# Kernel tuning notes

Measured on AMD Instinct MI355X. Metric: run time of the kernel, lower is better.

The kernel has to match this reference:

```python
import jax, jax.numpy as jnp
import numpy as np

H = 4
NEG_SLOPE = 0.2
N_P, N_A = 100000, 100000
E = 500000
L = 200000
F_IN, F_HID, F_OUT = 128, 128, 64


def setup_inputs() -> dict:
    key = jax.random.key(0)
    ks = jax.random.split(key, 32)
    s = 0.1  # weight init scale
    inp = {
        'x_paper': jax.random.normal(ks[0], (N_P, F_IN), jnp.float32),
        'x_author': jax.random.normal(ks[1], (N_A, F_IN), jnp.float32),
        'ei_pa': jax.random.randint(ks[2], (2, E), 0, N_P, jnp.int32),
        'ei_ap': jax.random.randint(ks[3], (2, E), 0, N_A, jnp.int32),
        'edge_label_index': jax.random.randint(ks[4], (2, L), 0, N_P, jnp.int32),
        # layer 1 params
        'p1W': s * jax.random.normal(ks[5], (F_IN, F_HID), jnp.float32),
        'p1b': jnp.zeros((F_HID,), jnp.float32),
        'a1W': s * jax.random.normal(ks[6], (F_IN, F_HID), jnp.float32),
        'a1b': jnp.zeros((F_HID,), jnp.float32),
        's1pa': s * jax.random.normal(ks[7], (H, F_HID // H), jnp.float32),
        'd1pa': s * jax.random.normal(ks[8], (H, F_HID // H), jnp.float32),
        's1ap': s * jax.random.normal(ks[9], (H, F_HID // H), jnp.float32),
        'd1ap': s * jax.random.normal(ks[10], (H, F_HID // H), jnp.float32),
        'k1W': s * jax.random.normal(ks[11], (F_HID, F_HID), jnp.float32),
        'k1b': jnp.zeros((F_HID,), jnp.float32),
        'q1': s * jax.random.normal(ks[12], (F_HID,), jnp.float32),
        # layer 2 params
        'p2W': s * jax.random.normal(ks[13], (F_HID, F_OUT), jnp.float32),
        'p2b': jnp.zeros((F_OUT,), jnp.float32),
        'a2W': s * jax.random.normal(ks[14], (F_HID, F_OUT), jnp.float32),
        'a2b': jnp.zeros((F_OUT,), jnp.float32),
        's2pa': s * jax.random.normal(ks[15], (H, F_OUT // H), jnp.float32),
        'd2pa': s * jax.random.normal(ks[16], (H, F_OUT // H), jnp.float32),
        's2ap': s * jax.random.normal(ks[17], (H, F_OUT // H), jnp.float32),
        'd2ap': s * jax.random.normal(ks[18], (H, F_OUT // H), jnp.float32),
        'k2W': s * jax.random.normal(ks[19], (F_OUT, F_OUT), jnp.float32),
        'k2b': jnp.zeros((F_OUT,), jnp.float32),
        'q2': s * jax.random.normal(ks[20], (F_OUT,), jnp.float32),
    }
    return inp


def _edge_attn(h_src, h_dst, src, dst, a_src, a_dst, num_dst):
    # h_*: [N, H, D]; a_*: [H, D]. Per-edge node-level GAT-style attention.
    alpha = (jnp.einsum('nhd,hd->nh', h_src, a_src)[src]
             + jnp.einsum('nhd,hd->nh', h_dst, a_dst)[dst])  # [E, H]
    alpha = jnp.where(alpha >= 0, alpha, NEG_SLOPE * alpha)  # leaky_relu
    amax = jax.ops.segment_max(alpha, dst, num_segments=num_dst)
    amax = jnp.where(jnp.isfinite(amax), amax, 0.0)
    ex = jnp.exp(alpha - amax[dst])
    denom = jax.ops.segment_sum(ex, dst, num_segments=num_dst)
    w = ex / (denom[dst] + 1e-16)
    out = jax.ops.segment_sum(h_src[src] * w[:, :, None], dst, num_segments=num_dst)
    return jax.nn.relu(out).reshape(num_dst, -1)  # [N_dst, H*D]


def _group(xs, q, kW, kb):
    # Semantic-level attention over metapaths (PyG HANConv `group`).
    out = jnp.stack(xs)  # [M, N, F]
    score = (q * jnp.tanh(out @ kW + kb).mean(axis=1)).sum(-1)  # [M]
    attn = jax.nn.softmax(score)
    return (attn[:, None, None] * out).sum(0)


def _han_layer(x_p, x_a, ei_pa, ei_ap, pW, pb, aW, ab, s_pa, d_pa, s_ap, d_ap, kW, kb, q):
    D = pW.shape[1] // H
    h_p = (x_p @ pW + pb).reshape(-1, H, D)
    h_a = (x_a @ aW + ab).reshape(-1, H, D)
    out_a = _edge_attn(h_p, h_a, ei_pa[0], ei_pa[1], s_pa, d_pa, h_a.shape[0])
    out_p = _edge_attn(h_a, h_p, ei_ap[0], ei_ap[1], s_ap, d_ap, h_p.shape[0])
    z_p = _group([out_p], q, kW, kb)
    z_a = _group([out_a], q, kW, kb)
    return z_p, z_a


def reference(x_paper, x_author, ei_pa, ei_ap, edge_label_index,
              p1W, p1b, a1W, a1b, s1pa, d1pa, s1ap, d1ap, k1W, k1b, q1,
              p2W, p2b, a2W, a2b, s2pa, d2pa, s2ap, d2ap, k2W, k2b, q2):
    z_p, z_a = _han_layer(x_paper, x_author, ei_pa, ei_ap,
                          p1W, p1b, a1W, a1b, s1pa, d1pa, s1ap, d1ap, k1W, k1b, q1)
    z_p, z_a = _han_layer(z_p, z_a, ei_pa, ei_ap,
                          p2W, p2b, a2W, a2b, s2pa, d2pa, s2ap, d2ap, k2W, k2b, q2)
    src = z_p[edge_label_index[0]]
    dst = z_a[edge_label_index[1]]
    return (src * dst).sum(axis=-1)  # [L]
```

## Files before the change

kernel.cpp:

```cpp
#include <hip/hip_runtime.h>


#define HEADS 4

typedef _Float16 f16x8 __attribute__((ext_vector_type(8)));
typedef _Float16 f16x4 __attribute__((ext_vector_type(4)));
typedef float    f32x4 __attribute__((ext_vector_type(4)));

__device__ __forceinline__ float leaky02(float a) {
    return a >= 0.f ? a : 0.2f * a;
}

__device__ __forceinline__ void prep_one(const float* W, _Float16* Wf, int M, int o) {
    const int v = o & 7, lane = (o >> 3) & 63, rest = o >> 9;
    const int jl = rest & 3, t = (rest >> 2) & 3, grp = rest >> 4;
    const int k = t * 32 + (lane >> 4) * 8 + v;
    const int n = (grp * 4 + jl) * 16 + (lane & 15);
    Wf[o] = (_Float16)W[k * M + n];
}

__global__ __launch_bounds__(256) void prep_w4(
    const float* __restrict__ W1, _Float16* __restrict__ Wf1,
    const float* __restrict__ W2, _Float16* __restrict__ Wf2,
    const float* __restrict__ W3, _Float16* __restrict__ Wf3,
    const float* __restrict__ W4, _Float16* __restrict__ Wf4) {
    int o = blockIdx.x * 256 + threadIdx.x;
    if (o < 16384)       prep_one(W1, Wf1, 128, o);
    else if (o < 32768)  prep_one(W2, Wf2, 128, o - 16384);
    else if (o < 40960)  prep_one(W3, Wf3, 64, o - 32768);
    else if (o < 49152)  prep_one(W4, Wf4, 64, o - 40960);
}

template<int M, bool AHALF>
__global__ __launch_bounds__(256) void gemm_mfma_dual(
    const void* __restrict__ XA, const _Float16* __restrict__ WfA,
    const float* __restrict__ bA, _Float16* __restrict__ outA,
    const float* __restrict__ svA, const float* __restrict__ dvA,
    float* __restrict__ asA, float* __restrict__ adA,
    const void* __restrict__ XB, const _Float16* __restrict__ WfB,
    const float* __restrict__ bB, _Float16* __restrict__ outB,
    const float* __restrict__ svB, const float* __restrict__ dvB,
    float* __restrict__ asB, float* __restrict__ adB,
    int N, int nbs) {
    constexpr int NSPLIT = (M == 128) ? 2 : 1;
    constexpr int JT  = 4;
    constexpr int D   = M / HEADS;
    constexpr int HPB = 64 / D;
    constexpr int HL  = 4 / HPB;
    constexpr int SA  = 136;
    constexpr int WFH = JT * 4 * 64 * 8;
    __shared__ _Float16 lds_a[64 * SA];
    __shared__ _Float16 lds_w[WFH];

    const bool second = blockIdx.x >= (unsigned)nbs;
    const void* __restrict__ X      = second ? XB : XA;
    const _Float16* __restrict__ Wf = second ? WfB : WfA;
    const float* __restrict__ b     = second ? bB : bA;
    _Float16* __restrict__ out      = second ? outB : outA;
    const float* __restrict__ sv    = second ? svB : svA;
    const float* __restrict__ dv    = second ? dvB : dvA;
    float* __restrict__ asb         = second ? asB : asA;
    float* __restrict__ adb         = second ? adB : adA;
    const int b0    = second ? blockIdx.x - nbs : blockIdx.x;
    const int brow  = b0 / NSPLIT;
    const int split = b0 % NSPLIT;
    const int row0  = brow * 64;
    const int colb  = split * 64;

    const int wave = threadIdx.x >> 6;
    const int lane = threadIdx.x & 63;
    const int m    = lane & 15;
    const int quad = lane >> 4;

    {
        const _Float16* wsrc = Wf + split * WFH;
        const int base = threadIdx.x * 8;
        #pragma unroll
        for (int it = 0; it < WFH / 2048; ++it) {
            f16x8 v = *(const f16x8*)(wsrc + it * 2048 + base);
            *(f16x8*)(lds_w + it * 2048 + base) = v;
        }
    }
    if (AHALF) {
        #pragma unroll
        for (int it = 0; it < 4; ++it) {
            const int r = it * 16 + (threadIdx.x >> 4);
            const int k = (threadIdx.x & 15) * 8;
            int gr = row0 + r; if (gr >= N) gr = N - 1;
            f16x8 v = *(const f16x8*)((const _Float16*)X + (size_t)gr * 128 + k);
            *(f16x8*)(lds_a + r * SA + k) = v;
        }
    } else {
        #pragma unroll
        for (int it = 0; it < 8; ++it) {
            const int r = it * 8 + (threadIdx.x >> 5);
            const int k = (threadIdx.x & 31) * 4;
            int gr = row0 + r; if (gr >= N) gr = N - 1;
            float4 v = *(const float4*)((const float*)X + (size_t)gr * 128 + k);
            f16x4 h = {(_Float16)v.x, (_Float16)v.y, (_Float16)v.z, (_Float16)v.w};
            *(f16x4*)(lds_a + r * SA + k) = h;
        }
    }
    __syncthreads();

    f32x4 acc[JT];
    #pragma unroll
    for (int j = 0; j < JT; ++j) acc[j] = (f32x4){0.f, 0.f, 0.f, 0.f};

    const int ab = (wave * 16 + m) * SA;
    #pragma unroll
    for (int t = 0; t < 4; ++t) {
        f16x8 a = *(const f16x8*)(lds_a + ab + t * 32 + quad * 8);
        #pragma unroll
        for (int j = 0; j < JT; ++j) {
            f16x8 bf = *(const f16x8*)(lds_w + ((t * JT + j) * 64 + lane) * 8);
            acc[j] = __builtin_amdgcn_mfma_f32_16x16x32_f16(a, bf, acc[j], 0, 0, 0);
        }
    }

    #pragma unroll
    for (int j = 0; j < JT; ++j) {
        const float bias = b[colb + j * 16 + m];
        #pragma unroll
        for (int r = 0; r < 4; ++r)
            lds_a[(wave * 16 + quad * 4 + r) * SA + j * 16 + m] =
                (_Float16)(acc[j][r] + bias);
    }

    {
        const int r = lane >> 2;
        const int q = lane & 3;
        float ps = 0.f, pd = 0.f;
        #pragma unroll
        for (int j = 0; j < 4; ++j) {
            f16x4 v4 = *(const f16x4*)(&lds_a[(wave * 16 + r) * SA + q * 16 + 4 * j]);
            float4 s4 = *(const float4*)(sv + colb + q * 16 + 4 * j);
            float4 d4 = *(const float4*)(dv + colb + q * 16 + 4 * j);
            const float v0 = (float)v4[0], v1 = (float)v4[1],
                        v2 = (float)v4[2], v3 = (float)v4[3];
            ps += v0 * s4.x + v1 * s4.y + v2 * s4.z + v3 * s4.w;
            pd += v0 * d4.x + v1 * d4.y + v2 * d4.z + v3 * d4.w;
        }
        if (HL == 2) { ps += __shfl_xor(ps, 1); pd += __shfl_xor(pd, 1); }
        const int grow = row0 + wave * 16 + r;
        if (grow < N && (q & (HL - 1)) == 0) {
            const int hh = split * HPB + q / HL;
            asb[(size_t)grow * HEADS + hh] = ps;
            adb[(size_t)grow * HEADS + hh] = pd;
        }
    }

    {
        const int lr = lane & 15;
        const int rq = lane >> 4;
        #pragma unroll
        for (int i = 0; i < 4; ++i) {
            const int lrow = i * 4 + rq;
            const int grow = row0 + wave * 16 + lrow;
            if (grow < N) {
                f16x4 v = *(const f16x4*)(&lds_a[(wave * 16 + lrow) * SA + lr * 4]);
                *(f16x4*)(out + (size_t)grow * M + colb + lr * 4) = v;
            }
        }
    }
}

__global__ __launch_bounds__(256) void hist_dual(
    const int* __restrict__ dst_pa, const int* __restrict__ dst_ap,
    int* __restrict__ counts, int N, int E) {
    const int eg = blockIdx.x * 256 + threadIdx.x;
    if (eg >= 2 * E) return;
    const int idx = (eg < E) ? dst_pa[eg] : (N + dst_ap[eg - E]);
    atomicAdd(counts + idx, 1);
}

__global__ __launch_bounds__(256) void scan_blk(
    const int* __restrict__ in, int* __restrict__ out,
    int* __restrict__ bsum, int N) {
    __shared__ int sh[256];
    const int base = blockIdx.x * 1024 + threadIdx.x * 4;
    int v[4]; int s = 0;
    #pragma unroll
    for (int j = 0; j < 4; ++j) { v[j] = (base + j < N) ? in[base + j] : 0; s += v[j]; }
    sh[threadIdx.x] = s;
    __syncthreads();
    for (int off = 1; off < 256; off <<= 1) {
        int t = (threadIdx.x >= off) ? sh[threadIdx.x - off] : 0;
        __syncthreads();
        sh[threadIdx.x] += t;
        __syncthreads();
    }
    int run = sh[threadIdx.x] - s;
    #pragma unroll
    for (int j = 0; j < 4; ++j) {
        if (base + j < N) out[base + j] = run;
        run += v[j];
    }
    if (threadIdx.x == 255) bsum[blockIdx.x] = sh[255];
}

__global__ __launch_bounds__(256) void scan_sums(int* __restrict__ bsum, int nb) {
    __shared__ int sh[256];
    int v = (threadIdx.x < nb) ? bsum[threadIdx.x] : 0;
    sh[threadIdx.x] = v;
    __syncthreads();
    for (int off = 1; off < 256; off <<= 1) {
        int t = (threadIdx.x >= off) ? sh[threadIdx.x - off] : 0;
        __syncthreads();
        sh[threadIdx.x] += t;
        __syncthreads();
    }
    if (threadIdx.x < nb) bsum[threadIdx.x] = sh[threadIdx.x] - v;
}

__global__ __launch_bounds__(256) void scan_add(
    int* __restrict__ out, const int* __restrict__ bsum, int N) {
    const int base = blockIdx.x * 1024 + threadIdx.x * 4;
    const int add = bsum[blockIdx.x];
    #pragma unroll
    for (int j = 0; j < 4; ++j)
        if (base + j < N) out[base + j] += add;
}

__global__ __launch_bounds__(256) void scatter_dual(
    const int* __restrict__ src_pa, const int* __restrict__ dst_pa,
    const int* __restrict__ src_ap, const int* __restrict__ dst_ap,
    const int* __restrict__ offsets, int* __restrict__ cursor,
    int* __restrict__ perm, int N, int E) {
    const int eg = blockIdx.x * 256 + threadIdx.x;
    if (eg >= 2 * E) return;
    int idx, val;
    if (eg < E) { idx = dst_pa[eg];         val = src_pa[eg]; }
    else        { idx = N + dst_ap[eg - E]; val = src_ap[eg - E]; }
    const int pos = offsets[idx] + atomicAdd(cursor + idx, 1);
    perm[pos] = val;
}

__global__ __launch_bounds__(256) void deg_hist(
    const int* __restrict__ cnt, int* __restrict__ bhist, int n) {
    __shared__ int lh[64];
    if (threadIdx.x < 64) lh[threadIdx.x] = 0;
    __syncthreads();
    for (int i = blockIdx.x * 256 + threadIdx.x; i < n; i += gridDim.x * 256) {
        int c = cnt[i]; if (c > 63) c = 63;
        atomicAdd(&lh[c], 1);
    }
    __syncthreads();
    if (threadIdx.x < 64) atomicAdd(&bhist[threadIdx.x], lh[threadIdx.x]);
}

__global__ __launch_bounds__(256) void deg_scatter(
    const int* __restrict__ cnt, int* __restrict__ bcur,
    int* __restrict__ order, int n) {
    __shared__ int lh[64];
    __shared__ int lbase[64];
    if (threadIdx.x < 64) lh[threadIdx.x] = 0;
    __syncthreads();
    const int i = blockIdx.x * 256 + threadIdx.x;
    int c = 0, lpos = 0;
    if (i < n) {
        c = cnt[i]; if (c > 63) c = 63;
        lpos = atomicAdd(&lh[c], 1);
    }
    __syncthreads();
    if (threadIdx.x < 64 && lh[threadIdx.x] > 0)
        lbase[threadIdx.x] = atomicAdd(&bcur[threadIdx.x], lh[threadIdx.x]);
    __syncthreads();
    if (i < n) order[lbase[c] + lpos] = i;
}

template<int F, int D>
__global__ __launch_bounds__(256) void csr_attn_agg_dual(
    const int* __restrict__ order,
    const int* __restrict__ perm, const int* __restrict__ offsets,
    const int* __restrict__ counts,
    const float* __restrict__ asrcP, const float* __restrict__ adstP,
    const _Float16* __restrict__ hP, _Float16* __restrict__ outA,
    const float* __restrict__ asrcA, const float* __restrict__ adstA,
    const _Float16* __restrict__ hA, _Float16* __restrict__ outP,
    int N) {
    constexpr int LPN = F / 8;
    const int gid  = blockIdx.x * 256 + threadIdx.x;
    const int slotF = gid / LPN;
    const int lane  = gid % LPN;
    if (slotF >= 2 * N) return;
    const int slot = 2 * N - 1 - slotF;
    const int node_g = order[slot];
    const bool second = node_g >= N;
    const int node = second ? node_g - N : node_g;
    const float* __restrict__ asrc    = second ? asrcA : asrcP;
    const float* __restrict__ adst    = second ? adstA : adstP;
    const _Float16* __restrict__ hsrc = second ? hA : hP;
    _Float16* __restrict__ out        = second ? outP : outA;

    const int start = offsets[node_g];
    const int cnt   = counts[node_g];
    const int f0 = lane * 8;
    const int h  = f0 / D;
    const float ad = adst[(size_t)node * HEADS + h];

    float den = 0.f;
    float acc[8];
    #pragma unroll
    for (int j = 0; j < 8; ++j) acc[j] = 0.f;
    const int last = cnt - 1;
    for (int i = 0; i < cnt; i += 4) {
        const int i1 = (i + 1 < cnt) ? i + 1 : last;
        const int i2 = (i + 2 < cnt) ? i + 2 : last;
        const int i3 = (i + 3 < cnt) ? i + 3 : last;
        const int s0 = perm[start + i];
        const int s1 = perm[start + i1];
        const int s2 = perm[start + i2];
        const int s3 = perm[start + i3];
        const float a0 = asrc[(size_t)s0 * HEADS + h];
        const float a1 = asrc[(size_t)s1 * HEADS + h];
        const float a2 = asrc[(size_t)s2 * HEADS + h];
        const float a3 = asrc[(size_t)s3 * HEADS + h];
        f16x8 h0 = *(const f16x8*)(hsrc + (size_t)s0 * F + f0);
        f16x8 h1 = *(const f16x8*)(hsrc + (size_t)s1 * F + f0);
        f16x8 h2 = *(const f16x8*)(hsrc + (size_t)s2 * F + f0);
        f16x8 h3 = *(const f16x8*)(hsrc + (size_t)s3 * F + f0);
        const float e0 = __expf(leaky02(a0 + ad));
        float e1 = __expf(leaky02(a1 + ad));
        float e2 = __expf(leaky02(a2 + ad));
        float e3 = __expf(leaky02(a3 + ad));
        if (i + 1 >= cnt) e1 = 0.f;
        if (i + 2 >= cnt) e2 = 0.f;
        if (i + 3 >= cnt) e3 = 0.f;
        den += (e0 + e1) + (e2 + e3);
        #pragma unroll
        for (int j = 0; j < 8; ++j)
            acc[j] += e0 * (float)h0[j] + e1 * (float)h1[j]
                    + e2 * (float)h2[j] + e3 * (float)h3[j];
    }
    const float inv = 1.f / (den + 1e-16f);
    f16x8 o;
    #pragma unroll
    for (int j = 0; j < 8; ++j)
        o[j] = (_Float16)fmaxf(acc[j] * inv, 0.f);
    *(f16x8*)(out + (size_t)node * F + f0) = o;
}

__global__ __launch_bounds__(256) void edge_dot(
    const int* __restrict__ eli, const _Float16* __restrict__ zp,
    const _Float16* __restrict__ za, float* __restrict__ out, int L) {
    constexpr int LPE = 8;
    const int gid  = blockIdx.x * blockDim.x + threadIdx.x;
    const int e    = gid / LPE;
    const int lane = gid % LPE;
    if (e >= L) return;
    const int p = eli[e], a = eli[(size_t)L + e];
    f16x8 pv = *(const f16x8*)(zp + (size_t)p * 64 + lane * 8);
    f16x8 av = *(const f16x8*)(za + (size_t)a * 64 + lane * 8);
    float s = 0.f;
    #pragma unroll
    for (int j = 0; j < 8; ++j) s += (float)pv[j] * (float)av[j];
    #pragma unroll
    for (int off = 4; off > 0; off >>= 1) s += __shfl_xor(s, off);
    if (lane == 0) out[e] = s;
}

static inline int cdiv(long long a, long long b) { return (int)((a + b - 1) / b); }

extern "C" void kernel_launch(void* const* d_in, const int* in_sizes, int n_in,
                              void* d_out, int out_size, void* d_ws, size_t ws_size,
                              hipStream_t stream) {
    const float* x_p  = (const float*)d_in[0];
    const float* x_a  = (const float*)d_in[1];
    const int* ei_pa  = (const int*)d_in[2];
    const int* ei_ap  = (const int*)d_in[3];
    const int* eli    = (const int*)d_in[4];
    const float* p1W = (const float*)d_in[5];
    const float* p1b = (const float*)d_in[6];
    const float* a1W = (const float*)d_in[7];
    const float* a1b = (const float*)d_in[8];
    const float* s1pa = (const float*)d_in[9];
    const float* d1pa = (const float*)d_in[10];
    const float* s1ap = (const float*)d_in[11];
    const float* d1ap = (const float*)d_in[12];
    const float* p2W = (const float*)d_in[16];
    const float* p2b = (const float*)d_in[17];
    const float* a2W = (const float*)d_in[18];
    const float* a2b = (const float*)d_in[19];
    const float* s2pa = (const float*)d_in[20];
    const float* d2pa = (const float*)d_in[21];
    const float* s2ap = (const float*)d_in[22];
    const float* d2ap = (const float*)d_in[23];

    const int NP = in_sizes[0] / 128;
    const int E  = in_sizes[2] / 2;
    const int L  = in_sizes[4] / 2;
    const int N  = NP;

    char* ws = (char*)d_ws;
    size_t off = 0;
    auto alloc = [&](size_t bytes) -> char* {
        char* p = ws + off;
        off += (bytes + 255) & ~(size_t)255;
        return p;
    };
    _Float16* h_p1   = (_Float16*)alloc((size_t)N * 128 * 2);
    _Float16* h_a1   = (_Float16*)alloc((size_t)N * 128 * 2);
    _Float16* out_p1 = (_Float16*)alloc((size_t)N * 128 * 2);
    _Float16* out_a1 = (_Float16*)alloc((size_t)N * 128 * 2);
    _Float16* h_p2   = (_Float16*)alloc((size_t)N * 64 * 2);
    _Float16* h_a2   = (_Float16*)alloc((size_t)N * 64 * 2);
    _Float16* out_p2 = (_Float16*)alloc((size_t)N * 64 * 2);
    _Float16* out_a2 = (_Float16*)alloc((size_t)N * 64 * 2);
    float* asrc_pa = (float*)alloc((size_t)N * HEADS * 4);
    float* adst_pa = (float*)alloc((size_t)N * HEADS * 4);
    float* asrc_ap = (float*)alloc((size_t)N * HEADS * 4);
    float* adst_ap = (float*)alloc((size_t)N * HEADS * 4);
    _Float16* Wf1p = (_Float16*)alloc(16384 * 2);
    _Float16* Wf1a = (_Float16*)alloc(16384 * 2);
    _Float16* Wf2p = (_Float16*)alloc(8192 * 2);
    _Float16* Wf2a = (_Float16*)alloc(8192 * 2);
    int* cnt2    = (int*)alloc((size_t)2 * N * 4);
    int* cursor2 = (int*)alloc((size_t)2 * N * 4);
    int* bhist   = (int*)alloc(256);
    int* off2    = (int*)alloc((size_t)2 * N * 4);
    int* perm2   = (int*)alloc((size_t)2 * E * 4);
    int* order2  = (int*)alloc((size_t)2 * N * 4);
    int* bsum    = (int*)alloc(256 * 4);

    const int* src_pa = ei_pa;
    const int* dst_pa = ei_pa + E;
    const int* src_ap = ei_ap;
    const int* dst_ap = ei_ap + E;

    const int N2 = 2 * N;
    const int nbScan = cdiv(N2, 1024);

    prep_w4<<<cdiv(49152, 256), 256, 0, stream>>>(p1W, Wf1p, a1W, Wf1a, p2W, Wf2p, a2W, Wf2a);
    hipMemsetAsync(cnt2, 0, ((size_t)4 * N + 64) * 4, stream);
    hist_dual<<<cdiv((long long)2 * E, 256), 256, 0, stream>>>(dst_pa, dst_ap, cnt2, N, E);
    scan_blk<<<nbScan, 256, 0, stream>>>(cnt2, off2, bsum, N2);
    scan_sums<<<1, 256, 0, stream>>>(bsum, nbScan);
    scan_add<<<nbScan, 256, 0, stream>>>(off2, bsum, N2);
    scatter_dual<<<cdiv((long long)2 * E, 256), 256, 0, stream>>>(
        src_pa, dst_pa, src_ap, dst_ap, off2, cursor2, perm2, N, E);
    deg_hist<<<256, 256, 0, stream>>>(cnt2, bhist, N2);
    scan_sums<<<1, 256, 0, stream>>>(bhist, 64);
    deg_scatter<<<cdiv(N2, 256), 256, 0, stream>>>(cnt2, bhist, order2, N2);

    const int nbs1 = cdiv(N, 64) * 2;
    const int nbs2 = cdiv(N, 64);

    gemm_mfma_dual<128, false><<<2 * nbs1, 256, 0, stream>>>(
        x_p, Wf1p, p1b, h_p1, s1pa, d1ap, asrc_pa, adst_ap,
        x_a, Wf1a, a1b, h_a1, s1ap, d1pa, asrc_ap, adst_pa, N, nbs1);
    csr_attn_agg_dual<128, 32><<<cdiv((long long)N2 * 16, 256), 256, 0, stream>>>(
        order2, perm2, off2, cnt2,
        asrc_pa, adst_pa, h_p1, out_a1,
        asrc_ap, adst_ap, h_a1, out_p1, N);

    gemm_mfma_dual<64, true><<<2 * nbs2, 256, 0, stream>>>(
        out_p1, Wf2p, p2b, h_p2, s2pa, d2ap, asrc_pa, adst_ap,
        out_a1, Wf2a, a2b, h_a2, s2ap, d2pa, asrc_ap, adst_pa, N, nbs2);
    csr_attn_agg_dual<64, 16><<<cdiv((long long)N2 * 8, 256), 256, 0, stream>>>(
        order2, perm2, off2, cnt2,
        asrc_pa, adst_pa, h_p2, out_a2,
        asrc_ap, adst_ap, h_a2, out_p2, N);

    edge_dot<<<cdiv((long long)L * 8, 256), 256, 0, stream>>>(
        eli, out_p2, out_a2, (float*)d_out, L);
}
```

Before: 439.5 us.

## Fuse layer-1 attention aggregation with layer-2 projection GEMM in one kernel

Replaces the layer-1 CSR attention aggregation kernel and the layer-2 projection GEMM with a single kernel. Each block aggregates 16 destination nodes, ordered by degree, into LDS, applies ReLU, multiplies by the LDS-resident layer-2 weights with MFMA, and writes h2 plus the per-head source and destination attention logits. This removes the out_p1/out_a1 intermediate round-trip through global memory and one launch. The degree-sort histogram now keeps paper and author nodes in separate buckets so each 16-node group belongs to one graph direction. The risks are load imbalance from the persistent grid-stride loop over groups, lower occupancy from the larger LDS footprint, and new attention-logit buffers.

```diff
diff --git a/kernel.cpp b/kernel.cpp
--- a/kernel.cpp
+++ b/kernel.cpp
@@ -237,36 +237,198 @@
 }
 
 __global__ __launch_bounds__(256) void deg_hist(
-    const int* __restrict__ cnt, int* __restrict__ bhist, int n) {
-    __shared__ int lh[64];
-    if (threadIdx.x < 64) lh[threadIdx.x] = 0;
-    __syncthreads();
-    for (int i = blockIdx.x * 256 + threadIdx.x; i < n; i += gridDim.x * 256) {
+    const int* __restrict__ cnt, int* __restrict__ bhist, int n2) {
+    __shared__ int lh[128];
+    if (threadIdx.x < 128) lh[threadIdx.x] = 0;
+    __syncthreads();
+    const int N = n2 >> 1;
+    for (int i = blockIdx.x * 256 + threadIdx.x; i < n2; i += gridDim.x * 256) {
         int c = cnt[i]; if (c > 63) c = 63;
-        atomicAdd(&lh[c], 1);
-    }
-    __syncthreads();
-    if (threadIdx.x < 64) atomicAdd(&bhist[threadIdx.x], lh[threadIdx.x]);
+        atomicAdd(&lh[(i >= N ? 64 : 0) + c], 1);
+    }
+    __syncthreads();
+    if (threadIdx.x < 128) atomicAdd(&bhist[threadIdx.x], lh[threadIdx.x]);
 }
 
 __global__ __launch_bounds__(256) void deg_scatter(
     const int* __restrict__ cnt, int* __restrict__ bcur,
-    int* __restrict__ order, int n) {
-    __shared__ int lh[64];
-    __shared__ int lbase[64];
-    if (threadIdx.x < 64) lh[threadIdx.x] = 0;
-    __syncthreads();
+    int* __restrict__ order, int n2) {
+    __shared__ int lh[128];
+    __shared__ int lbase[128];
+    if (threadIdx.x < 128) lh[threadIdx.x] = 0;
+    __syncthreads();
+    const int N = n2 >> 1;
     const int i = blockIdx.x * 256 + threadIdx.x;
-    int c = 0, lpos = 0;
-    if (i < n) {
-        c = cnt[i]; if (c > 63) c = 63;
-        lpos = atomicAdd(&lh[c], 1);
-    }
-    __syncthreads();
-    if (threadIdx.x < 64 && lh[threadIdx.x] > 0)
+    int key = 0, lpos = 0;
+    if (i < n2) {
+        int c = cnt[i]; if (c > 63) c = 63;
+        key = (i >= N ? 64 : 0) + c;
+        lpos = atomicAdd(&lh[key], 1);
+    }
+    __syncthreads();
+    if (threadIdx.x < 128 && lh[threadIdx.x] > 0)
         lbase[threadIdx.x] = atomicAdd(&bcur[threadIdx.x], lh[threadIdx.x]);
     __syncthreads();
-    if (i < n) order[lbase[c] + lpos] = i;
+    if (i < n2) order[lbase[key] + lpos] = i;
+}
+
+__global__ __launch_bounds__(256) void agg_proj_dual(
+    const int* __restrict__ order,
+    const int* __restrict__ perm, const int* __restrict__ offsets,
+    const int* __restrict__ counts,
+    const float* __restrict__ as1_0, const float* __restrict__ ad1_0,
+    const _Float16* __restrict__ h1_0,
+    const _Float16* __restrict__ Wf_0, const float* __restrict__ bb_0,
+    _Float16* __restrict__ h2_0,
+    const float* __restrict__ sv_0, const float* __restrict__ dv_0,
+    float* __restrict__ as2_0, float* __restrict__ ad2_0,
+    const float* __restrict__ as1_1, const float* __restrict__ ad1_1,
+    const _Float16* __restrict__ h1_1,
+    const _Float16* __restrict__ Wf_1, const float* __restrict__ bb_1,
+    _Float16* __restrict__ h2_1,
+    const float* __restrict__ sv_1, const float* __restrict__ dv_1,
+    float* __restrict__ as2_1, float* __restrict__ ad2_1,
+    int N, int GB) {
+    constexpr int SAF = 136;
+    constexpr int SH  = 72;
+    __shared__ _Float16 ldsW[8192];
+    __shared__ _Float16 ldsA[16 * SAF];
+    __shared__ _Float16 ldsH[16 * SH];
+
+    const bool d1 = blockIdx.x >= (unsigned)GB;
+    const float*    __restrict__ as1 = d1 ? as1_1 : as1_0;
+    const float*    __restrict__ ad1 = d1 ? ad1_1 : ad1_0;
+    const _Float16* __restrict__ h1  = d1 ? h1_1 : h1_0;
+    const _Float16* __restrict__ Wf  = d1 ? Wf_1 : Wf_0;
+    const float*    __restrict__ bb  = d1 ? bb_1 : bb_0;
+    _Float16*       __restrict__ h2  = d1 ? h2_1 : h2_0;
+    const float*    __restrict__ sv  = d1 ? sv_1 : sv_0;
+    const float*    __restrict__ dv  = d1 ? dv_1 : dv_0;
+    float*          __restrict__ as2 = d1 ? as2_1 : as2_0;
+    float*          __restrict__ ad2 = d1 ? ad2_1 : ad2_0;
+    const int b0    = d1 ? blockIdx.x - GB : blockIdx.x;
+    const int dbase = d1 ? N : 0;
+
+    const int tid  = threadIdx.x;
+    const int wave = tid >> 6;
+    const int lane = tid & 63;
+    const int nk   = tid >> 4;
+    const int fl   = tid & 15;
+    const int f0   = fl * 8;
+    const int hh   = fl >> 2;
+    const int m    = lane & 15;
+    const int quad = lane >> 4;
+
+    {
+        const int base = tid * 8;
+        #pragma unroll
+        for (int it = 0; it < 4; ++it) {
+            f16x8 v = *(const f16x8*)(Wf + it * 2048 + base);
+            *(f16x8*)(ldsW + it * 2048 + base) = v;
+        }
+    }
+
+    const int nG = (N + 15) >> 4;
+    for (int g = b0; g < nG; g += GB) {
+        f16x8 rowv;
+        #pragma unroll
+        for (int j = 0; j < 8; ++j) rowv[j] = (_Float16)0.f;
+        const int idx = g * 16 + nk;
+        if (idx < N) {
+            const int node_g = order[dbase + (N - 1 - idx)];
+            const int node   = node_g - dbase;
+            const int start  = offsets[node_g];
+            const int cnt    = counts[node_g];
+            const float ad   = ad1[(size_t)node * HEADS + hh];
+            float den = 0.f;
+            float acc[8];
+            #pragma unroll
+            for (int j = 0; j < 8; ++j) acc[j] = 0.f;
+            const int last = cnt - 1;
+            for (int i = 0; i < cnt; i += 4) {
+                const int i1 = (i + 1 < cnt) ? i + 1 : last;
+                const int i2 = (i + 2 < cnt) ? i + 2 : last;
+                const int i3 = (i + 3 < cnt) ? i + 3 : last;
+                const int s0 = perm[start + i];
+                const int s1 = perm[start + i1];
+                const int s2 = perm[start + i2];
+                const int s3 = perm[start + i3];
+                const float a0 = as1[(size_t)s0 * HEADS + hh];
+                const float a1 = as1[(size_t)s1 * HEADS + hh];
+                const float a2 = as1[(size_t)s2 * HEADS + hh];
+                const float a3 = as1[(size_t)s3 * HEADS + hh];
+                f16x8 h0 = *(const f16x8*)(h1 + (size_t)s0 * 128 + f0);
+                f16x8 hb = *(const f16x8*)(h1 + (size_t)s1 * 128 + f0);
+                f16x8 hc = *(const f16x8*)(h1 + (size_t)s2 * 128 + f0);
+                f16x8 hd = *(const f16x8*)(h1 + (size_t)s3 * 128 + f0);
+                const float e0 = __expf(leaky02(a0 + ad));
+                float e1 = __expf(leaky02(a1 + ad));
+                float e2 = __expf(leaky02(a2 + ad));
+                float e3 = __expf(leaky02(a3 + ad));
+                if (i + 1 >= cnt) e1 = 0.f;
+                if (i + 2 >= cnt) e2 = 0.f;
+                if (i + 3 >= cnt) e3 = 0.f;
+                den += (e0 + e1) + (e2 + e3);
+                #pragma unroll
+                for (int j = 0; j < 8; ++j)
+                    acc[j] += e0 * (float)h0[j] + e1 * (float)hb[j]
+                            + e2 * (float)hc[j] + e3 * (float)hd[j];
+            }
+            const float inv = 1.f / (den + 1e-16f);
+            #pragma unroll
+            for (int j = 0; j < 8; ++j)
+                rowv[j] = (_Float16)fmaxf(acc[j] * inv, 0.f);
+        }
+        *(f16x8*)(ldsA + nk * SAF + f0) = rowv;
+        __syncthreads();
+
+        f32x4 c = (f32x4){0.f, 0.f, 0.f, 0.f};
+        const int ab = m * SAF;
+        #pragma unroll
+        for (int t = 0; t < 4; ++t) {
+            f16x8 a  = *(const f16x8*)(ldsA + ab + t * 32 + quad * 8);
+            f16x8 bf = *(const f16x8*)(ldsW + ((t * 4 + wave) * 64 + lane) * 8);
+            c = __builtin_amdgcn_mfma_f32_16x16x32_f16(a, bf, c, 0, 0, 0);
+        }
+        const float bias = bb[wave * 16 + m];
+        #pragma unroll
+        for (int r = 0; r < 4; ++r)
+            ldsH[(quad * 4 + r) * SH + wave * 16 + m] = (_Float16)(c[r] + bias);
+        __syncthreads();
+
+        if (wave == 0) {
+            const int r = lane >> 2;
+            const int q = lane & 3;
+            const int aidx = g * 16 + r;
+            if (aidx < N) {
+                const int anode = order[dbase + (N - 1 - aidx)] - dbase;
+                float ps = 0.f, pd = 0.f;
+                #pragma unroll
+                for (int jj = 0; jj < 4; ++jj) {
+                    f16x4 v4 = *(const f16x4*)(&ldsH[r * SH + q * 16 + 4 * jj]);
+                    float4 s4 = *(const float4*)(sv + q * 16 + 4 * jj);
+                    float4 d4 = *(const float4*)(dv + q * 16 + 4 * jj);
+                    const float v0 = (float)v4[0], v1 = (float)v4[1],
+                                v2 = (float)v4[2], v3 = (float)v4[3];
+                    ps += v0 * s4.x + v1 * s4.y + v2 * s4.z + v3 * s4.w;
+                    pd += v0 * d4.x + v1 * d4.y + v2 * d4.z + v3 * d4.w;
+                }
+                as2[(size_t)anode * HEADS + q] = ps;
+                ad2[(size_t)anode * HEADS + q] = pd;
+            }
+        }
+        {
+            const int lr  = lane & 15;
+            const int rq  = lane >> 4;
+            const int row = wave * 4 + rq;
+            const int sidx = g * 16 + row;
+            if (sidx < N) {
+                const int snode = order[dbase + (N - 1 - sidx)] - dbase;
+                f16x4 v = *(const f16x4*)(&ldsH[row * SH + lr * 4]);
+                *(f16x4*)(h2 + (size_t)snode * 64 + lr * 4) = v;
+            }
+        }
+    }
 }
 
 template<int F, int D>
@@ -401,8 +563,6 @@
     };
     _Float16* h_p1   = (_Float16*)alloc((size_t)N * 128 * 2);
     _Float16* h_a1   = (_Float16*)alloc((size_t)N * 128 * 2);
-    _Float16* out_p1 = (_Float16*)alloc((size_t)N * 128 * 2);
-    _Float16* out_a1 = (_Float16*)alloc((size_t)N * 128 * 2);
     _Float16* h_p2   = (_Float16*)alloc((size_t)N * 64 * 2);
     _Float16* h_a2   = (_Float16*)alloc((size_t)N * 64 * 2);
     _Float16* out_p2 = (_Float16*)alloc((size_t)N * 64 * 2);
@@ -411,13 +571,17 @@
     float* adst_pa = (float*)alloc((size_t)N * HEADS * 4);
     float* asrc_ap = (float*)alloc((size_t)N * HEADS * 4);
     float* adst_ap = (float*)alloc((size_t)N * HEADS * 4);
+    float* as2_pa  = (float*)alloc((size_t)N * HEADS * 4);
+    float* ad2_pa  = (float*)alloc((size_t)N * HEADS * 4);
+    float* as2_ap  = (float*)alloc((size_t)N * HEADS * 4);
+    float* ad2_ap  = (float*)alloc((size_t)N * HEADS * 4);
     _Float16* Wf1p = (_Float16*)alloc(16384 * 2);
     _Float16* Wf1a = (_Float16*)alloc(16384 * 2);
     _Float16* Wf2p = (_Float16*)alloc(8192 * 2);
     _Float16* Wf2a = (_Float16*)alloc(8192 * 2);
     int* cnt2    = (int*)alloc((size_t)2 * N * 4);
     int* cursor2 = (int*)alloc((size_t)2 * N * 4);
-    int* bhist   = (int*)alloc(256);
+    int* bhist   = (int*)alloc(512);
     int* off2    = (int*)alloc((size_t)2 * N * 4);
     int* perm2   = (int*)alloc((size_t)2 * E * 4);
     int* order2  = (int*)alloc((size_t)2 * N * 4);
@@ -432,7 +596,7 @@
     const int nbScan = cdiv(N2, 1024);
 
     prep_w4<<<cdiv(49152, 256), 256, 0, stream>>>(p1W, Wf1p, a1W, Wf1a, p2W, Wf2p, a2W, Wf2a);
-    hipMemsetAsync(cnt2, 0, ((size_t)4 * N + 64) * 4, stream);
+    hipMemsetAsync(cnt2, 0, ((size_t)4 * N + 128) * 4, stream);
     hist_dual<<<cdiv((long long)2 * E, 256), 256, 0, stream>>>(dst_pa, dst_ap, cnt2, N, E);
     scan_blk<<<nbScan, 256, 0, stream>>>(cnt2, off2, bsum, N2);
     scan_sums<<<1, 256, 0, stream>>>(bsum, nbScan);
@@ -440,27 +604,27 @@
     scatter_dual<<<cdiv((long long)2 * E, 256), 256, 0, stream>>>(
         src_pa, dst_pa, src_ap, dst_ap, off2, cursor2, perm2, N, E);
     deg_hist<<<256, 256, 0, stream>>>(cnt2, bhist, N2);
-    scan_sums<<<1, 256, 0, stream>>>(bhist, 64);
+    scan_sums<<<1, 256, 0, stream>>>(bhist, 128);
     deg_scatter<<<cdiv(N2, 256), 256, 0, stream>>>(cnt2, bhist, order2, N2);
 
     const int nbs1 = cdiv(N, 64) * 2;
-    const int nbs2 = cdiv(N, 64);
 
     gemm_mfma_dual<128, false><<<2 * nbs1, 256, 0, stream>>>(
         x_p, Wf1p, p1b, h_p1, s1pa, d1ap, asrc_pa, adst_ap,
         x_a, Wf1a, a1b, h_a1, s1ap, d1pa, asrc_ap, adst_pa, N, nbs1);
-    csr_attn_agg_dual<128, 32><<<cdiv((long long)N2 * 16, 256), 256, 0, stream>>>(
+
+    const int nG = cdiv(N, 16);
+    const int GB = cdiv(nG, 10);
+    agg_proj_dual<<<2 * GB, 256, 0, stream>>>(
         order2, perm2, off2, cnt2,
-        asrc_pa, adst_pa, h_p1, out_a1,
-        asrc_ap, adst_ap, h_a1, out_p1, N);
-
-    gemm_mfma_dual<64, true><<<2 * nbs2, 256, 0, stream>>>(
-        out_p1, Wf2p, p2b, h_p2, s2pa, d2ap, asrc_pa, adst_ap,
-        out_a1, Wf2a, a2b, h_a2, s2ap, d2pa, asrc_ap, adst_pa, N, nbs2);
+        asrc_pa, adst_pa, h_p1, Wf2a, a2b, h_a2, s2ap, d2pa, as2_ap, ad2_pa,
+        asrc_ap, adst_ap, h_a1, Wf2p, p2b, h_p2, s2pa, d2ap, as2_pa, ad2_ap,
+        N, GB);
+
     csr_attn_agg_dual<64, 16><<<cdiv((long long)N2 * 8, 256), 256, 0, stream>>>(
         order2, perm2, off2, cnt2,
-        asrc_pa, adst_pa, h_p2, out_a2,
-        asrc_ap, adst_ap, h_a2, out_p2, N);
+        as2_pa, ad2_pa, h_p2, out_a2,
+        as2_ap, ad2_ap, h_a2, out_p2, N);
 
     edge_dot<<<cdiv((long long)L * 8, 256), 256, 0, stream>>>(
         eli, out_p2, out_a2, (float*)d_out, L);
```

Result: faster. 416.0 us (-5.3%).
